# Kernel tuning notes

Measured on AMD Instinct MI355X. Metric: run time of the kernel, lower is better.

Reference implementation:

```python
import jax, jax.numpy as jnp
import numpy as np

DIM = 1024
HEADS = 16
DH = DIM // HEADS          # 64
ROT_DIM = 2 * DH           # 128, rotary applied over concatenated x/a head dim
B, N = 2, 2048


def l2norm(t, eps=1e-12):
    # F.normalize(p=2, dim=-1)
    n = jnp.sqrt(jnp.sum(t * t, axis=-1, keepdims=True))
    return t / jnp.maximum(n, eps)


def rotate_half(t):
    t1, t2 = jnp.split(t, 2, axis=-1)
    return jnp.concatenate([-t2, t1], axis=-1)


def apply_rotary(q, k):
    # q: [b,h,n,ROT_DIM], k: [b,1,n,ROT_DIM]
    n = q.shape[-2]
    inv_freq = 1.0 / (10000.0 ** (jnp.arange(0, ROT_DIM, 2, dtype=jnp.float32) / ROT_DIM))
    freqs = jnp.outer(jnp.arange(n, dtype=jnp.float32), inv_freq)  # [n, ROT_DIM/2]
    emb = jnp.concatenate([freqs, freqs], axis=-1)                 # [n, ROT_DIM]
    cos, sin = jnp.cos(emb), jnp.sin(emb)
    q = q * cos + rotate_half(q) * sin
    k = k * cos + rotate_half(k) * sin
    return q, k


def setup_inputs() -> dict:
    key = jax.random.key(0)
    ks = jax.random.split(key, 6)
    s = 0.02
    return {
        "x": jax.random.normal(ks[0], (B, N, DIM), jnp.float32),
        "a": jax.random.normal(ks[1], (B, N, DIM), jnp.float32),
        "Wq_x": jax.random.normal(ks[2], (DIM, DIM), jnp.float32) * s,
        "Wkv_x": jax.random.normal(ks[3], (2 * DH, DIM), jnp.float32) * s,
        "Wq_a": jax.random.normal(ks[4], (DIM, DIM), jnp.float32) * s,
        "Wkv_a": jax.random.normal(ks[5], (2 * DH, DIM), jnp.float32) * s,
        "qx_scale": jnp.ones((HEADS, 1, DH), jnp.float32),
        "qa_scale": jnp.ones((HEADS, 1, DH), jnp.float32),
        "kx_scale": jnp.ones((1, 1, DH), jnp.float32),
        "ka_scale": jnp.ones((1, 1, DH), jnp.float32),
    }


def reference(x, a, Wq_x, Wkv_x, Wq_a, Wkv_a, qx_scale, qa_scale, kx_scale, ka_scale):
    b, n, _ = x.shape
    # q projections: [b,n,dim] -> [b,h,n,dh]
    q_x = (x @ Wq_x.T).reshape(b, n, HEADS, DH).transpose(0, 2, 1, 3)
    q_a = (a @ Wq_a.T).reshape(b, n, HEADS, DH).transpose(0, 2, 1, 3)
    # shared single KV head: [b,n,2*dh] -> two [b,1,n,dh]
    kv_x = x @ Wkv_x.T
    k_x, v_x = jnp.split(kv_x[:, None], 2, axis=-1)
    kv_a = a @ Wkv_a.T
    k_a, v_a = jnp.split(kv_a[:, None], 2, axis=-1)
    # qk-norm with learned per-head (q) / shared (k) scales
    q_x = l2norm(q_x) * qx_scale
    q_a = l2norm(q_a) * qa_scale
    k_x = l2norm(k_x) * kx_scale
    k_a = l2norm(k_a) * ka_scale
    # concat modalities along feature dim -> head dim 2*dh
    q = jnp.concatenate([q_x, q_a], axis=-1)   # [b,h,n,2dh]
    k = jnp.concatenate([k_x, k_a], axis=-1)   # [b,1,n,2dh]
    v = jnp.concatenate([v_x, v_a], axis=-1)   # [b,1,n,2dh]
    q, k = apply_rotary(q, k)
    # SDPA with broadcasted single KV head
    scale = 1.0 / jnp.sqrt(jnp.float32(ROT_DIM))
    k2, v2 = k[:, 0], v[:, 0]                  # [b,n,2dh]
    scores = jnp.einsum("bhqd,bkd->bhqk", q * scale, k2)
    attn = jax.nn.softmax(scores, axis=-1)
    out = jnp.einsum("bhqk,bkd->bhqd", attn, v2)  # [b,h,n,2dh]
    return out.transpose(0, 2, 1, 3).reshape(b, n, HEADS * ROT_DIM)
```

## Files before the change

kernel.cpp:

```cpp
#include <hip/hip_runtime.h>
#include <math.h>

#define DIM   1024
#define HEADS 16
#define DH    64
#define ROT   128
#define BATCH 2
#define SEQ   2048
#define ROWS  (BATCH*SEQ)
#define PCOLS (DIM + 2*DH)
#define ASCALE 0.08838834764831845f

typedef short bf16x8 __attribute__((ext_vector_type(8)));
typedef float f32x16 __attribute__((ext_vector_type(16)));

static __device__ __forceinline__ unsigned short f2bf(float f) {
    union { float f; unsigned u; } v; v.f = f;
    unsigned r = v.u + 0x7fffu + ((v.u >> 16) & 1u);
    return (unsigned short)(r >> 16);
}
static __device__ __forceinline__ float bf2f(unsigned short u) {
    union { unsigned u; float f; } v; v.u = (unsigned)u << 16;
    return v.f;
}

#define GL2LDS(gp, lp) __builtin_amdgcn_global_load_lds(                    \
    (const __attribute__((address_space(1))) void*)(gp),                    \
    (__attribute__((address_space(3))) void*)(lp), 16, 0, 0)

__global__ __launch_bounds__(256) void convert_kernel(
    const float* __restrict__ x, const float* __restrict__ a,
    const float* __restrict__ Wq_x, const float* __restrict__ Wkv_x,
    const float* __restrict__ Wq_a, const float* __restrict__ Wkv_a,
    unsigned short* __restrict__ xbf, unsigned short* __restrict__ wbf)
{
    const int blk = blockIdx.x;
    const float* s; unsigned short* d; int seg0;
    if      (blk < 1024) { s = x;     d = xbf;           seg0 = 0;    }
    else if (blk < 2048) { s = a;     d = xbf + 4194304; seg0 = 1024; }
    else if (blk < 2304) { s = Wq_x;  d = wbf;           seg0 = 2048; }
    else if (blk < 2336) { s = Wkv_x; d = wbf + 1048576; seg0 = 2304; }
    else if (blk < 2592) { s = Wq_a;  d = wbf + 1179648; seg0 = 2336; }
    else                 { s = Wkv_a; d = wbf + 2228224; seg0 = 2592; }
    long lb = ((long)blk - seg0) * 1024;
    #pragma unroll
    for (int j = 0; j < 4; j++) {
        long idx = lb + j * 256 + threadIdx.x;
        float4 v = ((const float4*)s)[idx];
        ((ushort4*)d)[idx] = make_ushort4(f2bf(v.x), f2bf(v.y), f2bf(v.z), f2bf(v.w));
    }
}

__global__ __launch_bounds__(256) void mfma_gemm_kernel(
    const unsigned short* __restrict__ xbf, const unsigned short* __restrict__ wbf,
    unsigned short* __restrict__ Pbf)
{
    const int mt = blockIdx.x, jt = blockIdx.y, side = blockIdx.z;
    const unsigned short* Ag = xbf + ((size_t)side * ROWS  + mt * 128) * DIM;
    const unsigned short* Bg = wbf + ((size_t)side * PCOLS + jt * 128) * DIM;
    unsigned short* Pp = Pbf + (size_t)side * ROWS * PCOLS;

    __shared__ __align__(16) unsigned short As[128 * 32];
    __shared__ __align__(16) unsigned short Bs[128 * 32];

    const int tid  = threadIdx.x;
    const int wave = tid >> 6, lane = tid & 63;
    const int m = lane & 31, hl = lane >> 5;
    const int wr = wave >> 1, wc = wave & 1;

    f32x16 acc[2][2];
    #pragma unroll
    for (int i2 = 0; i2 < 2; i2++)
        #pragma unroll
        for (int j2 = 0; j2 < 2; j2++) acc[i2][j2] = 0.0f;

    int sr[2], sg[2]; unsigned ldsb[2];
    #pragma unroll
    for (int it = 0; it < 2; it++) {
        int s = it * 256 + tid;
        sr[it] = s >> 2;
        sg[it] = (s & 3) ^ ((sr[it] >> 1) & 3);
        ldsb[it] = (unsigned)(it * 256 + wave * 64) * 16;
    }

    for (int k0 = 0; k0 < DIM; k0 += 32) {
        __syncthreads();
        #pragma unroll
        for (int it = 0; it < 2; it++) {
            GL2LDS(Ag + (size_t)sr[it] * DIM + k0 + sg[it] * 8, (char*)As + ldsb[it]);
            GL2LDS(Bg + (size_t)sr[it] * DIM + k0 + sg[it] * 8, (char*)Bs + ldsb[it]);
        }
        __syncthreads();
        #pragma unroll
        for (int kp = 0; kp < 2; kp++) {
            bf16x8 af[2], bff[2];
            #pragma unroll
            for (int t2 = 0; t2 < 2; t2++) {
                int ra = wr * 64 + t2 * 32 + m;
                int ga = (kp * 2 + hl) ^ ((ra >> 1) & 3);
                af[t2] = *(const bf16x8*)&As[ra * 32 + ga * 8];
                int rb = wc * 64 + t2 * 32 + m;
                int gb = (kp * 2 + hl) ^ ((rb >> 1) & 3);
                bff[t2] = *(const bf16x8*)&Bs[rb * 32 + gb * 8];
            }
            #pragma unroll
            for (int i2 = 0; i2 < 2; i2++)
                #pragma unroll
                for (int j2 = 0; j2 < 2; j2++)
                    acc[i2][j2] = __builtin_amdgcn_mfma_f32_32x32x16_bf16(
                        af[i2], bff[j2], acc[i2][j2], 0, 0, 0);
        }
    }

    const int m0 = mt * 128 + wr * 64;
    const int n0 = jt * 128 + wc * 64;
    #pragma unroll
    for (int i2 = 0; i2 < 2; i2++)
        #pragma unroll
        for (int j2 = 0; j2 < 2; j2++)
            #pragma unroll
            for (int r = 0; r < 16; r++) {
                int row = m0 + i2 * 32 + (r & 3) + 8 * (r >> 2) + 4 * hl;
                int col = n0 + j2 * 32 + m;
                Pp[(size_t)row * PCOLS + col] = f2bf(acc[i2][j2][r]);
            }
}

__global__ __launch_bounds__(256) void fuse_kernel(
    const unsigned short* __restrict__ Pbf,
    const float* __restrict__ qx_scale, const float* __restrict__ qa_scale,
    const float* __restrict__ kx_scale, const float* __restrict__ ka_scale,
    unsigned short* __restrict__ qbuf, unsigned short* __restrict__ kbuf,
    unsigned short* __restrict__ vbufT)
{
    const int row = blockIdx.x;
    const int b = row >> 11, pos = row & 2047;
    const unsigned short* Px = Pbf + (size_t)row * PCOLS;
    const unsigned short* Pa = Pbf + (size_t)ROWS * PCOLS + (size_t)row * PCOLS;
    const int tid = threadIdx.x;
    const int h = tid >> 4, i = tid & 15;
    const float fpos = (float)pos;
    const float LN1E4_64 = 0.14391156831213f;

    ushort4 xu = *(const ushort4*)(Px + h * DH + i * 4);
    ushort4 au = *(const ushort4*)(Pa + h * DH + i * 4);
    float xr[4] = {bf2f(xu.x), bf2f(xu.y), bf2f(xu.z), bf2f(xu.w)};
    float ar[4] = {bf2f(au.x), bf2f(au.y), bf2f(au.z), bf2f(au.w)};
    float ssx = xr[0]*xr[0] + xr[1]*xr[1] + xr[2]*xr[2] + xr[3]*xr[3];
    float ssa = ar[0]*ar[0] + ar[1]*ar[1] + ar[2]*ar[2] + ar[3]*ar[3];
    #pragma unroll
    for (int off = 1; off < 16; off <<= 1) {
        ssx += __shfl_xor(ssx, off, 16);
        ssa += __shfl_xor(ssa, off, 16);
    }
    float inx = 1.0f / fmaxf(sqrtf(ssx), 1e-12f);
    float ina = 1.0f / fmaxf(sqrtf(ssa), 1e-12f);
    unsigned short qlo[4], qhi[4];
    #pragma unroll
    for (int j = 0; j < 4; j++) {
        int jd = i * 4 + j;
        float qx = xr[j] * inx * qx_scale[h * DH + jd];
        float qa = ar[j] * ina * qa_scale[h * DH + jd];
        float th = fpos * expf(-LN1E4_64 * (float)jd);
        float sn, cs; sincosf(th, &sn, &cs);
        qlo[j] = f2bf((qx * cs - qa * sn) * ASCALE);
        qhi[j] = f2bf((qa * cs + qx * sn) * ASCALE);
    }
    unsigned short* qp = qbuf + (((size_t)(b * HEADS + h)) * SEQ + pos) * ROT;
    *(ushort4*)(qp + i * 4)      = make_ushort4(qlo[0], qlo[1], qlo[2], qlo[3]);
    *(ushort4*)(qp + DH + i * 4) = make_ushort4(qhi[0], qhi[1], qhi[2], qhi[3]);

    if (tid < 16) {
        ushort4 kxu = *(const ushort4*)(Px + DIM + tid * 4);
        ushort4 kau = *(const ushort4*)(Pa + DIM + tid * 4);
        float kxr[4] = {bf2f(kxu.x), bf2f(kxu.y), bf2f(kxu.z), bf2f(kxu.w)};
        float kar[4] = {bf2f(kau.x), bf2f(kau.y), bf2f(kau.z), bf2f(kau.w)};
        float sx = kxr[0]*kxr[0] + kxr[1]*kxr[1] + kxr[2]*kxr[2] + kxr[3]*kxr[3];
        float sa = kar[0]*kar[0] + kar[1]*kar[1] + kar[2]*kar[2] + kar[3]*kar[3];
        #pragma unroll
        for (int off = 1; off < 16; off <<= 1) {
            sx += __shfl_xor(sx, off, 16);
            sa += __shfl_xor(sa, off, 16);
        }
        float ikx = 1.0f / fmaxf(sqrtf(sx), 1e-12f);
        float ika = 1.0f / fmaxf(sqrtf(sa), 1e-12f);
        unsigned short klo[4], khi[4];
        #pragma unroll
        for (int j = 0; j < 4; j++) {
            int jd = tid * 4 + j;
            float kx = kxr[j] * ikx * kx_scale[jd];
            float ka = kar[j] * ika * ka_scale[jd];
            float th = fpos * expf(-LN1E4_64 * (float)jd);
            float sn, cs; sincosf(th, &sn, &cs);
            klo[j] = f2bf(kx * cs - ka * sn);
            khi[j] = f2bf(ka * cs + kx * sn);
        }
        unsigned short* kp = kbuf + ((size_t)b * SEQ + pos) * ROT;
        *(ushort4*)(kp + tid * 4)      = make_ushort4(klo[0], klo[1], klo[2], klo[3]);
        *(ushort4*)(kp + DH + tid * 4) = make_ushort4(khi[0], khi[1], khi[2], khi[3]);
    }
    if (tid >= 64 && tid < 96) {
        int iv = tid - 64;
        unsigned short* vT = vbufT + (size_t)b * ROT * SEQ + pos;
        const unsigned short* src; int d;
        if (iv < 16) { src = Px + DIM + DH + iv * 4;        d = iv * 4;              }
        else         { src = Pa + DIM + DH + (iv - 16) * 4; d = DH + (iv - 16) * 4;  }
        ushort4 v4 = *(const ushort4*)src;
        vT[(size_t)(d + 0) * SEQ] = v4.x;
        vT[(size_t)(d + 1) * SEQ] = v4.y;
        vT[(size_t)(d + 2) * SEQ] = v4.z;
        vT[(size_t)(d + 3) * SEQ] = v4.w;
    }
}

__global__ __launch_bounds__(256, 2) void attn_kernel(
    const unsigned short* __restrict__ qbuf,
    const unsigned short* __restrict__ kbuf,
    const unsigned short* __restrict__ vbufT,
    float* __restrict__ out)
{
    const int qb = blockIdx.x, h = blockIdx.y, b = blockIdx.z;
    __shared__ __align__(16) unsigned short Ks[64 * 128];
    __shared__ __align__(16) unsigned short Vs[128 * 64];
    const int tid  = threadIdx.x;
    const int wave = tid >> 6, lane = tid & 63;
    const int m = lane & 31, hl = lane >> 5;
    const int q0 = qb * 128 + wave * 32;

    bf16x8 qf[8];
    {
        const unsigned short* qp = qbuf + (((size_t)(b * HEADS + h)) * SEQ + q0 + m) * ROT + hl * 8;
        #pragma unroll
        for (int c = 0; c < 8; c++) qf[c] = *(const bf16x8*)(qp + c * 16);
    }

    f32x16 oacc[4];
    #pragma unroll
    for (int dt = 0; dt < 4; dt++) oacc[dt] = 0.0f;
    float lsum = 0.f;

    const unsigned short* kb_ = kbuf  + (size_t)b * SEQ * ROT;
    const unsigned short* vb_ = vbufT + (size_t)b * ROT * SEQ;

    for (int t = 0; t < SEQ / 64; t++) {
        __syncthreads();
        #pragma unroll
        for (int i = 0; i < 4; i++) {
            int fg = i * 256 + tid;
            int row = fg >> 4, gi = fg & 15;
            uint4 val = *(const uint4*)(kb_ + (size_t)(t * 64 + row) * ROT + gi * 8);
            *(uint4*)&Ks[row * 128 + ((gi ^ (row & 15)) << 3)] = val;
            int rv = fg >> 3, gv = fg & 7;
            uint4 vv = *(const uint4*)(vb_ + (size_t)rv * SEQ + t * 64 + gv * 8);
            *(uint4*)&Vs[rv * 64 + ((gv ^ (rv & 7)) << 3)] = vv;
        }
        __syncthreads();

        #pragma unroll
        for (int kg = 0; kg < 2; kg++) {
            f32x16 st = 0.0f;
            #pragma unroll
            for (int c = 0; c < 8; c++) {
                bf16x8 af = *(const bf16x8*)&Ks[(kg * 32 + m) * 128 + (((2 * c + hl) ^ (m & 15)) << 3)];
                st = __builtin_amdgcn_mfma_f32_32x32x16_bf16(af, qf[c], st, 0, 0, 0);
            }
            float p[16];
            #pragma unroll
            for (int r = 0; r < 16; r++) { p[r] = __expf(st[r]); lsum += p[r]; }

            #pragma unroll
            for (int w = 0; w < 2; w++) {
                float pj[8];
                #pragma unroll
                for (int tq = 0; tq < 4; tq++) {
                    float send = hl ? p[8 * w + tq]     : p[8 * w + 4 + tq];
                    float own  = hl ? p[8 * w + 4 + tq] : p[8 * w + tq];
                    float recv = __shfl_xor(send, 32);
                    pj[tq]     = hl ? recv : own;
                    pj[4 + tq] = hl ? own  : recv;
                }
                bf16x8 aP;
                #pragma unroll
                for (int j = 0; j < 8; j++) aP[j] = (short)f2bf(pj[j]);
                #pragma unroll
                for (int dt = 0; dt < 4; dt++) {
                    bf16x8 vf = *(const bf16x8*)&Vs[(dt * 32 + m) * 64 +
                                                    (((kg * 4 + w * 2 + hl) ^ (m & 7)) << 3)];
                    oacc[dt] = __builtin_amdgcn_mfma_f32_32x32x16_bf16(aP, vf, oacc[dt], 0, 0, 0);
                }
            }
        }
    }

    lsum += __shfl_xor(lsum, 32);
    float* ob = out + ((size_t)(b * SEQ + q0)) * (HEADS * ROT) + h * ROT + m;
    #pragma unroll
    for (int r = 0; r < 16; r++) {
        int qrow = (r & 3) + 8 * (r >> 2) + 4 * hl;
        float linv = 1.0f / __shfl(lsum, qrow);
        float* orow = ob + (size_t)qrow * (HEADS * ROT);
        #pragma unroll
        for (int dt = 0; dt < 4; dt++) orow[dt * 32] = oacc[dt][r] * linv;
    }
}

extern "C" void kernel_launch(void* const* d_in, const int* in_sizes, int n_in,
                              void* d_out, int out_size, void* d_ws, size_t ws_size,
                              hipStream_t stream) {
    (void)in_sizes; (void)n_in; (void)out_size; (void)ws_size;
    const float* x        = (const float*)d_in[0];
    const float* a        = (const float*)d_in[1];
    const float* Wq_x     = (const float*)d_in[2];
    const float* Wkv_x    = (const float*)d_in[3];
    const float* Wq_a     = (const float*)d_in[4];
    const float* Wkv_a    = (const float*)d_in[5];
    const float* qx_scale = (const float*)d_in[6];
    const float* qa_scale = (const float*)d_in[7];
    const float* kx_scale = (const float*)d_in[8];
    const float* ka_scale = (const float*)d_in[9];
    float* out = (float*)d_out;

    unsigned short* Pbf   = (unsigned short*)d_ws;
    unsigned short* qbuf  = Pbf   + (size_t)2 * ROWS * PCOLS;
    unsigned short* kbuf  = qbuf  + (size_t)BATCH * HEADS * SEQ * ROT;
    unsigned short* vbufT = kbuf  + (size_t)BATCH * SEQ * ROT;
    unsigned short* xbf   = vbufT + (size_t)BATCH * SEQ * ROT;
    unsigned short* wbf   = xbf   + (size_t)2 * ROWS * DIM;

    convert_kernel<<<dim3(2624), 256, 0, stream>>>(x, a, Wq_x, Wkv_x, Wq_a, Wkv_a, xbf, wbf);
    mfma_gemm_kernel<<<dim3(32, 9, 2), 256, 0, stream>>>(xbf, wbf, Pbf);
    fuse_kernel<<<dim3(ROWS), 256, 0, stream>>>(Pbf, qx_scale, qa_scale, kx_scale, ka_scale,
                                                qbuf, kbuf, vbufT);
    attn_kernel<<<dim3(SEQ / 128, HEADS, BATCH), 256, 0, stream>>>(qbuf, kbuf, vbufT, out);
}
```

Before: 240.3 us.

## Split attention KV across wave pairs, precompute rotary table, use direct LDS loads

The attention kernel now gives each block 64 queries instead of 128. Its four waves form two query tiles times two KV halves (split-K), and the partial outputs and row sums are merged through shared memory at the end. This doubles the grid and raises launch bounds to four blocks per SM for more occupancy. K tiles are loaded straight into LDS with global_load_lds, and V uses a new swizzle layout. Rotary sin/cos values are precomputed once into a table by extra blocks in the convert kernel, so the fuse kernel no longer calls sincos per head, at the cost of an extra table read and a combine step.

```diff
diff --git a/kernel.cpp b/kernel.cpp
--- a/kernel.cpp
+++ b/kernel.cpp
@@ -32,9 +32,24 @@
     const float* __restrict__ x, const float* __restrict__ a,
     const float* __restrict__ Wq_x, const float* __restrict__ Wkv_x,
     const float* __restrict__ Wq_a, const float* __restrict__ Wkv_a,
-    unsigned short* __restrict__ xbf, unsigned short* __restrict__ wbf)
+    unsigned short* __restrict__ xbf, unsigned short* __restrict__ wbf,
+    float2* __restrict__ tbl)
 {
     const int blk = blockIdx.x;
+    const float LN1E4_64 = 0.14391156831213f;
+    if (blk >= 2624) {
+        int local = blk - 2624;
+        int pos = local * 16 + (threadIdx.x >> 4);
+        int i   = threadIdx.x & 15;
+        #pragma unroll
+        for (int j = 0; j < 4; j++) {
+            int jd = i * 4 + j;
+            float th = (float)pos * expf(-LN1E4_64 * (float)jd);
+            float sn, cs; sincosf(th, &sn, &cs);
+            tbl[pos * 64 + jd] = make_float2(cs, sn);
+        }
+        return;
+    }
     const float* s; unsigned short* d; int seg0;
     if      (blk < 1024) { s = x;     d = xbf;           seg0 = 0;    }
     else if (blk < 2048) { s = a;     d = xbf + 4194304; seg0 = 1024; }
@@ -130,6 +145,7 @@
     const unsigned short* __restrict__ Pbf,
     const float* __restrict__ qx_scale, const float* __restrict__ qa_scale,
     const float* __restrict__ kx_scale, const float* __restrict__ ka_scale,
+    const float2* __restrict__ tbl,
     unsigned short* __restrict__ qbuf, unsigned short* __restrict__ kbuf,
     unsigned short* __restrict__ vbufT)
 {
@@ -139,8 +155,7 @@
     const unsigned short* Pa = Pbf + (size_t)ROWS * PCOLS + (size_t)row * PCOLS;
     const int tid = threadIdx.x;
     const int h = tid >> 4, i = tid & 15;
-    const float fpos = (float)pos;
-    const float LN1E4_64 = 0.14391156831213f;
+    const float2* tb = tbl + pos * 64;
 
     ushort4 xu = *(const ushort4*)(Px + h * DH + i * 4);
     ushort4 au = *(const ushort4*)(Pa + h * DH + i * 4);
@@ -161,10 +176,9 @@
         int jd = i * 4 + j;
         float qx = xr[j] * inx * qx_scale[h * DH + jd];
         float qa = ar[j] * ina * qa_scale[h * DH + jd];
-        float th = fpos * expf(-LN1E4_64 * (float)jd);
-        float sn, cs; sincosf(th, &sn, &cs);
-        qlo[j] = f2bf((qx * cs - qa * sn) * ASCALE);
-        qhi[j] = f2bf((qa * cs + qx * sn) * ASCALE);
+        float2 cssn = tb[jd];
+        qlo[j] = f2bf((qx * cssn.x - qa * cssn.y) * ASCALE);
+        qhi[j] = f2bf((qa * cssn.x + qx * cssn.y) * ASCALE);
     }
     unsigned short* qp = qbuf + (((size_t)(b * HEADS + h)) * SEQ + pos) * ROT;
     *(ushort4*)(qp + i * 4)      = make_ushort4(qlo[0], qlo[1], qlo[2], qlo[3]);
@@ -190,10 +204,9 @@
             int jd = tid * 4 + j;
             float kx = kxr[j] * ikx * kx_scale[jd];
             float ka = kar[j] * ika * ka_scale[jd];
-            float th = fpos * expf(-LN1E4_64 * (float)jd);
-            float sn, cs; sincosf(th, &sn, &cs);
-            klo[j] = f2bf(kx * cs - ka * sn);
-            khi[j] = f2bf(ka * cs + kx * sn);
+            float2 cssn = tb[jd];
+            klo[j] = f2bf(kx * cssn.x - ka * cssn.y);
+            khi[j] = f2bf(ka * cssn.x + kx * cssn.y);
         }
         unsigned short* kp = kbuf + ((size_t)b * SEQ + pos) * ROT;
         *(ushort4*)(kp + tid * 4)      = make_ushort4(klo[0], klo[1], klo[2], klo[3]);
@@ -213,19 +226,24 @@
     }
 }
 
-__global__ __launch_bounds__(256, 2) void attn_kernel(
+__global__ __launch_bounds__(256, 4) void attn_kernel(
     const unsigned short* __restrict__ qbuf,
     const unsigned short* __restrict__ kbuf,
     const unsigned short* __restrict__ vbufT,
     float* __restrict__ out)
 {
     const int qb = blockIdx.x, h = blockIdx.y, b = blockIdx.z;
-    __shared__ __align__(16) unsigned short Ks[64 * 128];
-    __shared__ __align__(16) unsigned short Vs[128 * 64];
+    __shared__ __align__(16) char smem[33280];
     const int tid  = threadIdx.x;
     const int wave = tid >> 6, lane = tid & 63;
+    const int qt = wave & 1, ks = wave >> 1;
     const int m = lane & 31, hl = lane >> 5;
-    const int q0 = qb * 128 + wave * 32;
+    const int q0 = qb * 64 + qt * 32;
+
+    unsigned short* KsAll = (unsigned short*)smem;
+    unsigned short* VsAll = (unsigned short*)(smem + 16384);
+    unsigned short* Ks = KsAll + ks * 4096;
+    unsigned short* Vs = VsAll + ks * 4096;
 
     bf16x8 qf[8];
     {
@@ -242,65 +260,85 @@
     const unsigned short* kb_ = kbuf  + (size_t)b * SEQ * ROT;
     const unsigned short* vb_ = vbufT + (size_t)b * ROT * SEQ;
 
-    for (int t = 0; t < SEQ / 64; t++) {
+    for (int t = 0; t < 32; t++) {
         __syncthreads();
         #pragma unroll
-        for (int i = 0; i < 4; i++) {
-            int fg = i * 256 + tid;
-            int row = fg >> 4, gi = fg & 15;
-            uint4 val = *(const uint4*)(kb_ + (size_t)(t * 64 + row) * ROT + gi * 8);
-            *(uint4*)&Ks[row * 128 + ((gi ^ (row & 15)) << 3)] = val;
-            int rv = fg >> 3, gv = fg & 7;
-            uint4 vv = *(const uint4*)(vb_ + (size_t)rv * SEQ + t * 64 + gv * 8);
-            *(uint4*)&Vs[rv * 64 + ((gv ^ (rv & 7)) << 3)] = vv;
+        for (int it = 0; it < 4; it++) {
+            int s = it * 256 + tid;
+            int set = s >> 9, krow = (s >> 4) & 31, kg = s & 15;
+            int kgg = kg ^ (krow & 15);
+            int kt = set * 1024 + t * 32;
+            GL2LDS(kb_ + (size_t)(kt + krow) * ROT + kgg * 8,
+                   (char*)KsAll + (unsigned)(it * 256 + wave * 64) * 16);
+            int d = (s >> 2) & 127, vg = s & 3;
+            int vgg = vg ^ ((d >> 1) & 3);
+            uint4 vv = *(const uint4*)(vb_ + (size_t)d * SEQ + kt + vgg * 8);
+            *(uint4*)&VsAll[(size_t)s * 8] = vv;
         }
         __syncthreads();
 
-        #pragma unroll
-        for (int kg = 0; kg < 2; kg++) {
-            f32x16 st = 0.0f;
-            #pragma unroll
-            for (int c = 0; c < 8; c++) {
-                bf16x8 af = *(const bf16x8*)&Ks[(kg * 32 + m) * 128 + (((2 * c + hl) ^ (m & 15)) << 3)];
-                st = __builtin_amdgcn_mfma_f32_32x32x16_bf16(af, qf[c], st, 0, 0, 0);
+        f32x16 st = 0.0f;
+        #pragma unroll
+        for (int c = 0; c < 8; c++) {
+            bf16x8 af = *(const bf16x8*)&Ks[m * 128 + (((2 * c + hl) ^ (m & 15)) << 3)];
+            st = __builtin_amdgcn_mfma_f32_32x32x16_bf16(af, qf[c], st, 0, 0, 0);
+        }
+        float p[16];
+        #pragma unroll
+        for (int r = 0; r < 16; r++) { p[r] = __expf(st[r]); lsum += p[r]; }
+
+        #pragma unroll
+        for (int w = 0; w < 2; w++) {
+            float pj[8];
+            #pragma unroll
+            for (int tq = 0; tq < 4; tq++) {
+                float send = hl ? p[8 * w + tq]     : p[8 * w + 4 + tq];
+                float own  = hl ? p[8 * w + 4 + tq] : p[8 * w + tq];
+                float recv = __shfl_xor(send, 32);
+                pj[tq]     = hl ? recv : own;
+                pj[4 + tq] = hl ? own  : recv;
             }
-            float p[16];
-            #pragma unroll
-            for (int r = 0; r < 16; r++) { p[r] = __expf(st[r]); lsum += p[r]; }
-
-            #pragma unroll
-            for (int w = 0; w < 2; w++) {
-                float pj[8];
-                #pragma unroll
-                for (int tq = 0; tq < 4; tq++) {
-                    float send = hl ? p[8 * w + tq]     : p[8 * w + 4 + tq];
-                    float own  = hl ? p[8 * w + 4 + tq] : p[8 * w + tq];
-                    float recv = __shfl_xor(send, 32);
-                    pj[tq]     = hl ? recv : own;
-                    pj[4 + tq] = hl ? own  : recv;
-                }
-                bf16x8 aP;
-                #pragma unroll
-                for (int j = 0; j < 8; j++) aP[j] = (short)f2bf(pj[j]);
-                #pragma unroll
-                for (int dt = 0; dt < 4; dt++) {
-                    bf16x8 vf = *(const bf16x8*)&Vs[(dt * 32 + m) * 64 +
-                                                    (((kg * 4 + w * 2 + hl) ^ (m & 7)) << 3)];
-                    oacc[dt] = __builtin_amdgcn_mfma_f32_32x32x16_bf16(aP, vf, oacc[dt], 0, 0, 0);
-                }
+            bf16x8 aP;
+            #pragma unroll
+            for (int j = 0; j < 8; j++) aP[j] = (short)f2bf(pj[j]);
+            #pragma unroll
+            for (int dt = 0; dt < 4; dt++) {
+                int d = dt * 32 + m;
+                bf16x8 vf = *(const bf16x8*)&Vs[d * 32 + (((2 * w + hl) ^ ((d >> 1) & 3)) << 3)];
+                oacc[dt] = __builtin_amdgcn_mfma_f32_32x32x16_bf16(aP, vf, oacc[dt], 0, 0, 0);
             }
         }
     }
 
-    lsum += __shfl_xor(lsum, 32);
-    float* ob = out + ((size_t)(b * SEQ + q0)) * (HEADS * ROT) + h * ROT + m;
-    #pragma unroll
-    for (int r = 0; r < 16; r++) {
-        int qrow = (r & 3) + 8 * (r >> 2) + 4 * hl;
-        float linv = 1.0f / __shfl(lsum, qrow);
-        float* orow = ob + (size_t)qrow * (HEADS * ROT);
-        #pragma unroll
-        for (int dt = 0; dt < 4; dt++) orow[dt * 32] = oacc[dt][r] * linv;
+    __syncthreads();
+    float* cb = (float*)smem;
+    if (ks == 1) {
+        float* dst = cb + (size_t)(qt * 64 + lane) * 65;
+        #pragma unroll
+        for (int dt = 0; dt < 4; dt++)
+            #pragma unroll
+            for (int r = 0; r < 16; r++) dst[dt * 16 + r] = oacc[dt][r];
+        dst[64] = lsum;
+    }
+    __syncthreads();
+    if (ks == 0) {
+        const float* src = cb + (size_t)(qt * 64 + lane) * 65;
+        #pragma unroll
+        for (int dt = 0; dt < 4; dt++)
+            #pragma unroll
+            for (int r = 0; r < 16; r++) oacc[dt][r] += src[dt * 16 + r];
+        lsum += src[64];
+        lsum += __shfl_xor(lsum, 32);
+
+        float* ob = out + ((size_t)(b * SEQ + q0)) * (HEADS * ROT) + h * ROT + m;
+        #pragma unroll
+        for (int r = 0; r < 16; r++) {
+            int qrow = (r & 3) + 8 * (r >> 2) + 4 * hl;
+            float linv = 1.0f / __shfl(lsum, qrow);
+            float* orow = ob + (size_t)qrow * (HEADS * ROT);
+            #pragma unroll
+            for (int dt = 0; dt < 4; dt++) orow[dt * 32] = oacc[dt][r] * linv;
+        }
     }
 }
 
@@ -326,10 +364,12 @@
     unsigned short* vbufT = kbuf  + (size_t)BATCH * SEQ * ROT;
     unsigned short* xbf   = vbufT + (size_t)BATCH * SEQ * ROT;
     unsigned short* wbf   = xbf   + (size_t)2 * ROWS * DIM;
-
-    convert_kernel<<<dim3(2624), 256, 0, stream>>>(x, a, Wq_x, Wkv_x, Wq_a, Wkv_a, xbf, wbf);
+    float2*         tbl   = (float2*)(wbf + (size_t)2 * PCOLS * DIM);
+
+    convert_kernel<<<dim3(2752), 256, 0, stream>>>(x, a, Wq_x, Wkv_x, Wq_a, Wkv_a,
+                                                   xbf, wbf, tbl);
     mfma_gemm_kernel<<<dim3(32, 9, 2), 256, 0, stream>>>(xbf, wbf, Pbf);
     fuse_kernel<<<dim3(ROWS), 256, 0, stream>>>(Pbf, qx_scale, qa_scale, kx_scale, ka_scale,
-                                                qbuf, kbuf, vbufT);
-    attn_kernel<<<dim3(SEQ / 128, HEADS, BATCH), 256, 0, stream>>>(qbuf, kbuf, vbufT, out);
-}
+                                                tbl, qbuf, kbuf, vbufT);
+    attn_kernel<<<dim3(SEQ / 64, HEADS, BATCH), 256, 0, stream>>>(qbuf, kbuf, vbufT, out);
+}
```

Measured after the change: 311.9 us. 1.3x slower.
